# Performance work log

Measured on AMD Instinct MI355X. Metric: run time of the kernel, lower is better.

Reference implementation:

```python
import jax, jax.numpy as jnp
import numpy as np

B, S, E, H = 2, 2048, 1024, 16
D = E // H  # head dim = 64


def setup_inputs() -> dict:
    key = jax.random.key(0)
    ks = jax.random.split(key, 8)
    s = 1.0 / np.sqrt(E)  # keep projections well-scaled
    return {
        "query": jax.random.normal(ks[0], (B, S, E), jnp.float32),
        "key": jax.random.normal(ks[1], (B, S, E), jnp.float32),
        "value": jax.random.normal(ks[2], (B, S, E), jnp.float32),
        "Wq": jax.random.normal(ks[3], (E, E), jnp.float32) * s,
        "bq": jnp.zeros((E,), jnp.float32),
        "Wk": jax.random.normal(ks[4], (E, E), jnp.float32) * s,
        "bk": jnp.zeros((E,), jnp.float32),
        "Wv": jax.random.normal(ks[5], (E, E), jnp.float32) * s,
        "bv": jnp.zeros((E,), jnp.float32),
        "Wo": jax.random.normal(ks[6], (E, E), jnp.float32) * s,
        "bo": jnp.zeros((E,), jnp.float32),
    }


def _split_heads(x):
    # (b, s, h*d) -> (b, h, s, d)
    b, s, _ = x.shape
    return x.reshape(b, s, H, D).transpose(0, 2, 1, 3)


def reference(query, key, value, Wq, bq, Wk, bk, Wv, bv, Wo, bo):
    # Linear projections (torch Linear: x @ W^T + b)
    q = _split_heads(query @ Wq.T + bq)  # (b, h, s_q, d)
    k = _split_heads(key @ Wk.T + bk)    # (b, h, s_k, d)
    v = _split_heads(value @ Wv.T + bv)  # (b, h, s_k, d)
    # scaled dot-product attention; scale uses head dim of key
    scores = jnp.einsum("bhqd,bhkd->bhqk", q, k) * (D ** -0.5)
    attn = jax.nn.softmax(scores, axis=-1)  # (b, h, s_q, s_k)
    ctx = jnp.einsum("bhqk,bhkd->bhqd", attn, v)
    # merge heads: (b, h, s, d) -> (b, s, h*d)
    ctx = ctx.transpose(0, 2, 1, 3).reshape(B, S, H * D)
    out = ctx @ Wo.T + bo  # (b, s, out_dim)
    return out, attn
```

## Files before the change

### kernel.cpp

```cpp
#include <hip/hip_runtime.h>

typedef _Float16 f16;
typedef _Float16 f16x4 __attribute__((ext_vector_type(4)));
typedef _Float16 f16x8 __attribute__((ext_vector_type(8)));
typedef float f32x4 __attribute__((ext_vector_type(4)));

#define S_LEN 2048
#define EMB 1024
#define NH 16
#define HD 64
#define BATCH 2

__device__ __forceinline__ void gload_lds16(const void* g, void* l) {
  __builtin_amdgcn_global_load_lds(
      (const __attribute__((address_space(1))) void*)g,
      (__attribute__((address_space(3))) void*)l, 16, 0, 0);
}

__global__ __launch_bounds__(256) void cast_kernel(const float* __restrict__ in,
                                                   f16* __restrict__ out, int n4) {
  int i = blockIdx.x * 256 + threadIdx.x;
  if (i >= n4) return;
  const float4 v = reinterpret_cast<const float4*>(in)[i];
  f16x4 o;
  o[0] = (f16)v.x; o[1] = (f16)v.y; o[2] = (f16)v.z; o[3] = (f16)v.w;
  reinterpret_cast<f16x4*>(out)[i] = o;
}

template <int MODE>
__global__ __launch_bounds__(256) void gemm_bt(const f16* __restrict__ A,
                                               const f16* __restrict__ Bw,
                                               const float* __restrict__ bias,
                                               void* __restrict__ outp,
                                               int M, int N, int K) {
  __shared__ f16 As[128 * 64];
  __shared__ f16 Bs[64 * 64];
  const int tid = threadIdx.x;
  const int w = tid >> 6, lane = tid & 63;
  const int lg = lane >> 4, l15 = lane & 15;
  const int m0 = blockIdx.y * 128, n0 = blockIdx.x * 64;
  f32x4 acc[2][4] = {};
  for (int k0 = 0; k0 < K; k0 += 64) {
#pragma unroll
    for (int i = 0; i < 4; i++) {
      int c = i * 4 + w, o = c * 64 + lane;
      gload_lds16(A + (size_t)(m0 + (o >> 3)) * K + k0 + ((o & 7) << 3), As + c * 512);
    }
#pragma unroll
    for (int i = 0; i < 2; i++) {
      int c = i * 4 + w, o = c * 64 + lane;
      gload_lds16(Bw + (size_t)(n0 + (o >> 3)) * K + k0 + ((o & 7) << 3), Bs + c * 512);
    }
    __syncthreads();
#pragma unroll
    for (int kk = 0; kk < 2; kk++) {
      f16x8 af[2], bf[4];
#pragma unroll
      for (int mi = 0; mi < 2; mi++)
        af[mi] = *(const f16x8*)&As[(w * 32 + mi * 16 + l15) * 64 + kk * 32 + lg * 8];
#pragma unroll
      for (int ni = 0; ni < 4; ni++)
        bf[ni] = *(const f16x8*)&Bs[(ni * 16 + l15) * 64 + kk * 32 + lg * 8];
#pragma unroll
      for (int mi = 0; mi < 2; mi++)
#pragma unroll
        for (int ni = 0; ni < 4; ni++)
          acc[mi][ni] =
              __builtin_amdgcn_mfma_f32_16x16x32_f16(af[mi], bf[ni], acc[mi][ni], 0, 0, 0);
    }
    __syncthreads();
  }
#pragma unroll
  for (int mi = 0; mi < 2; mi++)
#pragma unroll
    for (int ni = 0; ni < 4; ni++) {
      const int gn = n0 + ni * 16 + l15;
      const float bv = bias[gn];
#pragma unroll
      for (int r = 0; r < 4; r++) {
        const int gm = m0 + w * 32 + mi * 16 + lg * 4 + r;
        const float v = acc[mi][ni][r] + bv;
        if (MODE == 1) {
          ((float*)outp)[(size_t)gm * N + gn] = v;
        } else {
          const int b = gm >> 11, s = gm & 2047;
          const int h = gn >> 6, d = gn & 63;
          if (MODE == 0)
            ((f16*)outp)[(((size_t)(b * NH + h)) * S_LEN + s) * HD + d] = (f16)v;
          else
            ((f16*)outp)[(((size_t)(b * NH + h)) * HD + d) * S_LEN + s] = (f16)v;
        }
      }
    }
}

__global__ __launch_bounds__(256) void attn_kernel(const f16* __restrict__ Qp,
                                                   const f16* __restrict__ Kp,
                                                   const f16* __restrict__ VtG,
                                                   float* __restrict__ attn_out,
                                                   f16* __restrict__ ctx_out) {
  __shared__ f16 Vt[64 * 128];
  __shared__ f16 Ps[4][16 * 136];
  const int tid = threadIdx.x;
  const int w = tid >> 6, lane = tid & 63;
  const int lg = lane >> 4, l15 = lane & 15;
  const int bh = blockIdx.y;
  const int b = bh >> 4, h = bh & 15;
  const int q0 = blockIdx.x * 64;
  const f16* Qbh = Qp + (size_t)bh * S_LEN * HD;
  const f16* Kbh = Kp + (size_t)bh * S_LEN * HD;
  const f16* Vtbh = VtG + (size_t)bh * HD * S_LEN;
  const int qrow_base = q0 + w * 16;

  f16x8 qf[2];
  const f16 qsc = (f16)0.18033688f;
#pragma unroll
  for (int kk = 0; kk < 2; kk++) {
    qf[kk] = *(const f16x8*)&Qbh[(size_t)(qrow_base + l15) * HD + kk * 32 + lg * 8];
#pragma unroll
    for (int j = 0; j < 8; j++) qf[kk][j] *= qsc;
  }

  float m2[4], l[4];
#pragma unroll
  for (int r = 0; r < 4; r++) { m2[r] = -1e30f; l[r] = 0.f; }

  for (int kt = 0; kt < S_LEN; kt += 128) {
    f32x4 sf[8] = {};
#pragma unroll
    for (int kk = 0; kk < 2; kk++)
#pragma unroll
      for (int nf = 0; nf < 8; nf++) {
        f16x8 kf = *(const f16x8*)&Kbh[(size_t)(kt + nf * 16 + l15) * HD + kk * 32 + lg * 8];
        sf[nf] = __builtin_amdgcn_mfma_f32_16x16x32_f16(qf[kk], kf, sf[nf], 0, 0, 0);
      }
#pragma unroll
    for (int r = 0; r < 4; r++) {
      float pm = sf[0][r];
#pragma unroll
      for (int nf = 1; nf < 8; nf++) pm = fmaxf(pm, sf[nf][r]);
#pragma unroll
      for (int ofs = 1; ofs < 16; ofs <<= 1) pm = fmaxf(pm, __shfl_xor(pm, ofs));
      const float mn = fmaxf(m2[r], pm);
      float ps = 0.f;
#pragma unroll
      for (int nf = 0; nf < 8; nf++) ps += exp2f(sf[nf][r] - mn);
#pragma unroll
      for (int ofs = 1; ofs < 16; ofs <<= 1) ps += __shfl_xor(ps, ofs);
      l[r] = l[r] * exp2f(m2[r] - mn) + ps;
      m2[r] = mn;
    }
  }
#pragma unroll
  for (int r = 0; r < 4; r++) m2[r] += log2f(l[r]);

#define STAGE_LOAD(KT)                                                      \
  {                                                                         \
    _Pragma("unroll") for (int c = 0; c < 4; c++) {                         \
      const int idx = c * 256 + tid;                                        \
      const int rr = idx >> 4, bb = idx & 15;                               \
      vreg[c] = *(const f16x8*)&Vtbh[(size_t)rr * S_LEN + (KT) + bb * 8];   \
    }                                                                       \
  }
#define STAGE_WRITE()                                                       \
  {                                                                         \
    _Pragma("unroll") for (int c = 0; c < 4; c++) {                         \
      const int idx = c * 256 + tid;                                        \
      const int rr = idx >> 4, bb = idx & 15;                               \
      *(f16x8*)((char*)Vt + rr * 256 + ((bb ^ (rr & 7)) << 4)) = vreg[c];   \
    }                                                                       \
  }

  f32x4 cacc[4] = {};
  f16x8 vreg[4];
  STAGE_LOAD(0);
  STAGE_WRITE();
  asm volatile("s_waitcnt lgkmcnt(0)\n\ts_barrier" ::: "memory");

  for (int t = 0; t < 16; t++) {
    const int kt = t * 128;
    STAGE_LOAD(((t + 1) & 15) * 128);

    f32x4 sf[8] = {};
#pragma unroll
    for (int kk = 0; kk < 2; kk++)
#pragma unroll
      for (int nf = 0; nf < 8; nf++) {
        f16x8 kf = *(const f16x8*)&Kbh[(size_t)(kt + nf * 16 + l15) * HD + kk * 32 + lg * 8];
        sf[nf] = __builtin_amdgcn_mfma_f32_16x16x32_f16(qf[kk], kf, sf[nf], 0, 0, 0);
      }
#pragma unroll
    for (int nf = 0; nf < 8; nf++)
#pragma unroll
      for (int r = 0; r < 4; r++) {
        const float p = exp2f(sf[nf][r] - m2[r]);
        const int qrow = qrow_base + lg * 4 + r;
        attn_out[((size_t)bh * S_LEN + qrow) * S_LEN + kt + nf * 16 + l15] = p;
        Ps[w][(lg * 4 + r) * 136 + nf * 16 + l15] = (f16)p;
      }
#pragma unroll
    for (int kk2 = 0; kk2 < 4; kk2++) {
      f16x8 pf = *(const f16x8*)&Ps[w][l15 * 136 + kk2 * 32 + lg * 8];
#pragma unroll
      for (int nf2 = 0; nf2 < 4; nf2++) {
        const int rr = nf2 * 16 + l15, bb = kk2 * 4 + lg;
        f16x8 vf = *(const f16x8*)((const char*)Vt + rr * 256 + ((bb ^ (rr & 7)) << 4));
        cacc[nf2] = __builtin_amdgcn_mfma_f32_16x16x32_f16(pf, vf, cacc[nf2], 0, 0, 0);
      }
    }
    asm volatile("s_barrier" ::: "memory");
    STAGE_WRITE();
    asm volatile("s_waitcnt lgkmcnt(0)\n\ts_barrier" ::: "memory");
  }
#pragma unroll
  for (int nf2 = 0; nf2 < 4; nf2++)
#pragma unroll
    for (int r = 0; r < 4; r++) {
      const int qrow = qrow_base + lg * 4 + r;
      const int gr = b * S_LEN + qrow;
      const int gc = h * HD + nf2 * 16 + l15;
      ctx_out[(size_t)gr * EMB + gc] = (f16)cacc[nf2][r];
    }
#undef STAGE_LOAD
#undef STAGE_WRITE
}

extern "C" void kernel_launch(void* const* d_in, const int* in_sizes, int n_in,
                              void* d_out, int out_size, void* d_ws, size_t ws_size,
                              hipStream_t stream) {
  const float* query = (const float*)d_in[0];
  const float* key_i = (const float*)d_in[1];
  const float* value = (const float*)d_in[2];
  const float* Wq = (const float*)d_in[3];
  const float* bq = (const float*)d_in[4];
  const float* Wk = (const float*)d_in[5];
  const float* bk = (const float*)d_in[6];
  const float* Wv = (const float*)d_in[7];
  const float* bv = (const float*)d_in[8];
  const float* Wo = (const float*)d_in[9];
  const float* bo = (const float*)d_in[10];

  float* out = (float*)d_out;
  float* attn = out + (size_t)BATCH * S_LEN * EMB;

  f16* ws = (f16*)d_ws;
  const size_t NTOK = (size_t)BATCH * S_LEN;
  f16* Qh = ws;
  f16* Kh = Qh + NTOK * EMB;
  f16* Vh = Kh + NTOK * EMB;
  f16* Wqh = Vh + NTOK * EMB;
  f16* Wkh = Wqh + (size_t)EMB * EMB;
  f16* Wvh = Wkh + (size_t)EMB * EMB;
  f16* Woh = Wvh + (size_t)EMB * EMB;
  f16* Qp = Woh + (size_t)EMB * EMB;
  f16* Kp = Qp + NTOK * EMB;
  f16* VtG = Kp + NTOK * EMB;
  f16* ctx = VtG + NTOK * EMB;

  const int n4_x = (int)(NTOK * EMB / 4);
  const int n4_w = (int)((size_t)EMB * EMB / 4);
  cast_kernel<<<n4_x / 256, 256, 0, stream>>>(query, Qh, n4_x);
  cast_kernel<<<n4_x / 256, 256, 0, stream>>>(key_i, Kh, n4_x);
  cast_kernel<<<n4_x / 256, 256, 0, stream>>>(value, Vh, n4_x);
  cast_kernel<<<n4_w / 256, 256, 0, stream>>>(Wq, Wqh, n4_w);
  cast_kernel<<<n4_w / 256, 256, 0, stream>>>(Wk, Wkh, n4_w);
  cast_kernel<<<n4_w / 256, 256, 0, stream>>>(Wv, Wvh, n4_w);
  cast_kernel<<<n4_w / 256, 256, 0, stream>>>(Wo, Woh, n4_w);

  dim3 ggrid(EMB / 64, (unsigned)(NTOK / 128));
  gemm_bt<0><<<ggrid, 256, 0, stream>>>(Qh, Wqh, bq, Qp, (int)NTOK, EMB, EMB);
  gemm_bt<0><<<ggrid, 256, 0, stream>>>(Kh, Wkh, bk, Kp, (int)NTOK, EMB, EMB);
  gemm_bt<2><<<ggrid, 256, 0, stream>>>(Vh, Wvh, bv, VtG, (int)NTOK, EMB, EMB);

  attn_kernel<<<dim3(S_LEN / 64, BATCH * NH), 256, 0, stream>>>(Qp, Kp, VtG, attn, ctx);

  gemm_bt<1><<<ggrid, 256, 0, stream>>>(ctx, Woh, bo, out, (int)NTOK, EMB, EMB);
}
```

Measured before the change: 970.1 us.

## Transpose score MFMA operands for vectorized attn writes and shrink GEMM tiles

The attention kernel swaps the MFMA operand order so each lane holds four consecutive key columns of one query row. This allows float4 stores of the attention matrix, packed f16x4 writes to the P staging buffer, and a softmax reduction with only two cross-lane shuffles. The GEMM tile shrinks from 128x64 to 64x64, doubling the grid, and the transposed V projection now writes packed f16x4 along the sequence axis. The smaller tile gives more blocks but less operand reuse per block.

```diff
diff --git a/kernel.cpp b/kernel.cpp
--- a/kernel.cpp
+++ b/kernel.cpp
@@ -33,65 +33,61 @@
                                                const float* __restrict__ bias,
                                                void* __restrict__ outp,
                                                int M, int N, int K) {
-  __shared__ f16 As[128 * 64];
+  __shared__ f16 As[64 * 64];
   __shared__ f16 Bs[64 * 64];
   const int tid = threadIdx.x;
   const int w = tid >> 6, lane = tid & 63;
   const int lg = lane >> 4, l15 = lane & 15;
-  const int m0 = blockIdx.y * 128, n0 = blockIdx.x * 64;
-  f32x4 acc[2][4] = {};
+  const int m0 = blockIdx.y * 64, n0 = blockIdx.x * 64;
+  f32x4 acc[4] = {};
   for (int k0 = 0; k0 < K; k0 += 64) {
 #pragma unroll
-    for (int i = 0; i < 4; i++) {
+    for (int i = 0; i < 2; i++) {
       int c = i * 4 + w, o = c * 64 + lane;
       gload_lds16(A + (size_t)(m0 + (o >> 3)) * K + k0 + ((o & 7) << 3), As + c * 512);
-    }
-#pragma unroll
-    for (int i = 0; i < 2; i++) {
-      int c = i * 4 + w, o = c * 64 + lane;
       gload_lds16(Bw + (size_t)(n0 + (o >> 3)) * K + k0 + ((o & 7) << 3), Bs + c * 512);
     }
     __syncthreads();
 #pragma unroll
     for (int kk = 0; kk < 2; kk++) {
-      f16x8 af[2], bf[4];
-#pragma unroll
-      for (int mi = 0; mi < 2; mi++)
-        af[mi] = *(const f16x8*)&As[(w * 32 + mi * 16 + l15) * 64 + kk * 32 + lg * 8];
+      f16x8 af = *(const f16x8*)&As[(w * 16 + l15) * 64 + kk * 32 + lg * 8];
+      f16x8 bf[4];
 #pragma unroll
       for (int ni = 0; ni < 4; ni++)
         bf[ni] = *(const f16x8*)&Bs[(ni * 16 + l15) * 64 + kk * 32 + lg * 8];
 #pragma unroll
-      for (int mi = 0; mi < 2; mi++)
-#pragma unroll
-        for (int ni = 0; ni < 4; ni++)
-          acc[mi][ni] =
-              __builtin_amdgcn_mfma_f32_16x16x32_f16(af[mi], bf[ni], acc[mi][ni], 0, 0, 0);
+      for (int ni = 0; ni < 4; ni++)
+        acc[ni] = __builtin_amdgcn_mfma_f32_16x16x32_f16(af, bf[ni], acc[ni], 0, 0, 0);
     }
     __syncthreads();
   }
 #pragma unroll
-  for (int mi = 0; mi < 2; mi++)
-#pragma unroll
-    for (int ni = 0; ni < 4; ni++) {
-      const int gn = n0 + ni * 16 + l15;
-      const float bv = bias[gn];
+  for (int ni = 0; ni < 4; ni++) {
+    const int gn = n0 + ni * 16 + l15;
+    const float bv = bias[gn];
+    if (MODE == 2) {
+      const int gm0 = m0 + w * 16 + lg * 4;
+      const int b = gm0 >> 11, s0 = gm0 & 2047;
+      const int h = gn >> 6, d = gn & 63;
+      f16x4 pk;
+#pragma unroll
+      for (int r = 0; r < 4; r++) pk[r] = (f16)(acc[ni][r] + bv);
+      *(f16x4*)&((f16*)outp)[(((size_t)(b * NH + h)) * HD + d) * S_LEN + s0] = pk;
+    } else {
 #pragma unroll
       for (int r = 0; r < 4; r++) {
-        const int gm = m0 + w * 32 + mi * 16 + lg * 4 + r;
-        const float v = acc[mi][ni][r] + bv;
+        const int gm = m0 + w * 16 + lg * 4 + r;
+        const float v = acc[ni][r] + bv;
         if (MODE == 1) {
           ((float*)outp)[(size_t)gm * N + gn] = v;
         } else {
           const int b = gm >> 11, s = gm & 2047;
           const int h = gn >> 6, d = gn & 63;
-          if (MODE == 0)
-            ((f16*)outp)[(((size_t)(b * NH + h)) * S_LEN + s) * HD + d] = (f16)v;
-          else
-            ((f16*)outp)[(((size_t)(b * NH + h)) * HD + d) * S_LEN + s] = (f16)v;
+          ((f16*)outp)[(((size_t)(b * NH + h)) * S_LEN + s) * HD + d] = (f16)v;
         }
       }
     }
+  }
 }
 
 __global__ __launch_bounds__(256) void attn_kernel(const f16* __restrict__ Qp,
@@ -110,20 +106,18 @@
   const f16* Qbh = Qp + (size_t)bh * S_LEN * HD;
   const f16* Kbh = Kp + (size_t)bh * S_LEN * HD;
   const f16* Vtbh = VtG + (size_t)bh * HD * S_LEN;
-  const int qrow_base = q0 + w * 16;
+  const int qrow = q0 + w * 16 + l15;
 
   f16x8 qf[2];
   const f16 qsc = (f16)0.18033688f;
 #pragma unroll
   for (int kk = 0; kk < 2; kk++) {
-    qf[kk] = *(const f16x8*)&Qbh[(size_t)(qrow_base + l15) * HD + kk * 32 + lg * 8];
+    qf[kk] = *(const f16x8*)&Qbh[(size_t)qrow * HD + kk * 32 + lg * 8];
 #pragma unroll
     for (int j = 0; j < 8; j++) qf[kk][j] *= qsc;
   }
 
-  float m2[4], l[4];
-#pragma unroll
-  for (int r = 0; r < 4; r++) { m2[r] = -1e30f; l[r] = 0.f; }
+  float m2 = -1e30f, l = 0.f;
 
   for (int kt = 0; kt < S_LEN; kt += 128) {
     f32x4 sf[8] = {};
@@ -132,27 +126,27 @@
 #pragma unroll
       for (int nf = 0; nf < 8; nf++) {
         f16x8 kf = *(const f16x8*)&Kbh[(size_t)(kt + nf * 16 + l15) * HD + kk * 32 + lg * 8];
-        sf[nf] = __builtin_amdgcn_mfma_f32_16x16x32_f16(qf[kk], kf, sf[nf], 0, 0, 0);
-      }
-#pragma unroll
-    for (int r = 0; r < 4; r++) {
-      float pm = sf[0][r];
-#pragma unroll
-      for (int nf = 1; nf < 8; nf++) pm = fmaxf(pm, sf[nf][r]);
-#pragma unroll
-      for (int ofs = 1; ofs < 16; ofs <<= 1) pm = fmaxf(pm, __shfl_xor(pm, ofs));
-      const float mn = fmaxf(m2[r], pm);
-      float ps = 0.f;
-#pragma unroll
-      for (int nf = 0; nf < 8; nf++) ps += exp2f(sf[nf][r] - mn);
-#pragma unroll
-      for (int ofs = 1; ofs < 16; ofs <<= 1) ps += __shfl_xor(ps, ofs);
-      l[r] = l[r] * exp2f(m2[r] - mn) + ps;
-      m2[r] = mn;
-    }
-  }
-#pragma unroll
-  for (int r = 0; r < 4; r++) m2[r] += log2f(l[r]);
+        sf[nf] = __builtin_amdgcn_mfma_f32_16x16x32_f16(kf, qf[kk], sf[nf], 0, 0, 0);
+      }
+    float pm = sf[0][0];
+#pragma unroll
+    for (int nf = 0; nf < 8; nf++)
+#pragma unroll
+      for (int r = 0; r < 4; r++) pm = fmaxf(pm, sf[nf][r]);
+    pm = fmaxf(pm, __shfl_xor(pm, 16));
+    pm = fmaxf(pm, __shfl_xor(pm, 32));
+    const float mn = fmaxf(m2, pm);
+    float ps = 0.f;
+#pragma unroll
+    for (int nf = 0; nf < 8; nf++)
+#pragma unroll
+      for (int r = 0; r < 4; r++) ps += exp2f(sf[nf][r] - mn);
+    ps += __shfl_xor(ps, 16);
+    ps += __shfl_xor(ps, 32);
+    l = l * exp2f(m2 - mn) + ps;
+    m2 = mn;
+  }
+  m2 += log2f(l);
 
 #define STAGE_LOAD(KT)                                                      \
   {                                                                         \
@@ -177,6 +171,8 @@
   STAGE_WRITE();
   asm volatile("s_waitcnt lgkmcnt(0)\n\ts_barrier" ::: "memory");
 
+  float* arow_base = attn_out + ((size_t)bh * S_LEN + qrow) * S_LEN + lg * 4;
+
   for (int t = 0; t < 16; t++) {
     const int kt = t * 128;
     STAGE_LOAD(((t + 1) & 15) * 128);
@@ -187,17 +183,20 @@
 #pragma unroll
       for (int nf = 0; nf < 8; nf++) {
         f16x8 kf = *(const f16x8*)&Kbh[(size_t)(kt + nf * 16 + l15) * HD + kk * 32 + lg * 8];
-        sf[nf] = __builtin_amdgcn_mfma_f32_16x16x32_f16(qf[kk], kf, sf[nf], 0, 0, 0);
-      }
-#pragma unroll
-    for (int nf = 0; nf < 8; nf++)
-#pragma unroll
-      for (int r = 0; r < 4; r++) {
-        const float p = exp2f(sf[nf][r] - m2[r]);
-        const int qrow = qrow_base + lg * 4 + r;
-        attn_out[((size_t)bh * S_LEN + qrow) * S_LEN + kt + nf * 16 + l15] = p;
-        Ps[w][(lg * 4 + r) * 136 + nf * 16 + l15] = (f16)p;
-      }
+        sf[nf] = __builtin_amdgcn_mfma_f32_16x16x32_f16(kf, qf[kk], sf[nf], 0, 0, 0);
+      }
+#pragma unroll
+    for (int nf = 0; nf < 8; nf++) {
+      float4 pv;
+      pv.x = exp2f(sf[nf][0] - m2);
+      pv.y = exp2f(sf[nf][1] - m2);
+      pv.z = exp2f(sf[nf][2] - m2);
+      pv.w = exp2f(sf[nf][3] - m2);
+      *(float4*)&arow_base[kt + nf * 16] = pv;
+      f16x4 ph;
+      ph[0] = (f16)pv.x; ph[1] = (f16)pv.y; ph[2] = (f16)pv.z; ph[3] = (f16)pv.w;
+      *(f16x4*)&Ps[w][l15 * 136 + nf * 16 + lg * 4] = ph;
+    }
 #pragma unroll
     for (int kk2 = 0; kk2 < 4; kk2++) {
       f16x8 pf = *(const f16x8*)&Ps[w][l15 * 136 + kk2 * 32 + lg * 8];
@@ -216,8 +215,8 @@
   for (int nf2 = 0; nf2 < 4; nf2++)
 #pragma unroll
     for (int r = 0; r < 4; r++) {
-      const int qrow = qrow_base + lg * 4 + r;
-      const int gr = b * S_LEN + qrow;
+      const int qr = q0 + w * 16 + lg * 4 + r;
+      const int gr = b * S_LEN + qr;
       const int gc = h * HD + nf2 * 16 + l15;
       ctx_out[(size_t)gr * EMB + gc] = (f16)cacc[nf2][r];
     }
@@ -267,7 +266,7 @@
   cast_kernel<<<n4_w / 256, 256, 0, stream>>>(Wv, Wvh, n4_w);
   cast_kernel<<<n4_w / 256, 256, 0, stream>>>(Wo, Woh, n4_w);
 
-  dim3 ggrid(EMB / 64, (unsigned)(NTOK / 128));
+  dim3 ggrid(EMB / 64, (unsigned)(NTOK / 64));
   gemm_bt<0><<<ggrid, 256, 0, stream>>>(Qh, Wqh, bq, Qp, (int)NTOK, EMB, EMB);
   gemm_bt<0><<<ggrid, 256, 0, stream>>>(Kh, Wkh, bk, Kp, (int)NTOK, EMB, EMB);
   gemm_bt<2><<<ggrid, 256, 0, stream>>>(Vh, Wvh, bv, VtG, (int)NTOK, EMB, EMB);
```

Measured after the change: 1.068 ms. 10.0% more time.

## Batch QKV projections into one launch with 128x128 GEMM tiles

Applied to the files above, without the earlier changes.

Replaces the 128x64 GEMM with a 128x128 tile kernel where each wave computes a 64x64 sub-tile, which doubles operand reuse per LDS load. The three Q/K/V projections become one launch, with the grid column index selecting the input, weight and output, so there are fewer launches and more blocks per launch. The transposed V output is now written as packed f16x4 vector stores. Each thread holds twice the accumulators, which raises register pressure and can lower occupancy. The output projection gets half as many blocks as before.

```diff
diff --git a/kernel.cpp b/kernel.cpp
--- a/kernel.cpp
+++ b/kernel.cpp
@@ -27,19 +27,31 @@
   reinterpret_cast<f16x4*>(out)[i] = o;
 }
 
-template <int MODE>
-__global__ __launch_bounds__(256) void gemm_bt(const f16* __restrict__ A,
-                                               const f16* __restrict__ Bw,
-                                               const float* __restrict__ bias,
-                                               void* __restrict__ outp,
-                                               int M, int N, int K) {
+template <int OUT>
+__global__ __launch_bounds__(256) void gemm128(
+    const f16* __restrict__ A0, const f16* __restrict__ A1, const f16* __restrict__ A2,
+    const f16* __restrict__ B0, const f16* __restrict__ B1, const f16* __restrict__ B2,
+    const float* __restrict__ b0, const float* __restrict__ b1, const float* __restrict__ b2,
+    void* o0, void* o1, void* o2, int K) {
   __shared__ f16 As[128 * 64];
-  __shared__ f16 Bs[64 * 64];
-  const int tid = threadIdx.x;
-  const int w = tid >> 6, lane = tid & 63;
+  __shared__ f16 Bs[128 * 64];
+  const int tid = threadIdx.x, w = tid >> 6, lane = tid & 63;
   const int lg = lane >> 4, l15 = lane & 15;
-  const int m0 = blockIdx.y * 128, n0 = blockIdx.x * 64;
-  f32x4 acc[2][4] = {};
+  const int wr = w >> 1, wc = w & 1;
+  const int m0 = blockIdx.y * 128;
+  const int n0g = blockIdx.x * 128;
+  const f16 *A, *Bw;
+  const float* bias;
+  int sel, n0;
+  if (OUT == 0) {
+    sel = n0g >> 10; n0 = n0g & 1023;
+    A = sel == 0 ? A0 : (sel == 1 ? A1 : A2);
+    Bw = sel == 0 ? B0 : (sel == 1 ? B1 : B2);
+    bias = sel == 0 ? b0 : (sel == 1 ? b1 : b2);
+  } else {
+    sel = 0; n0 = n0g; A = A0; Bw = B0; bias = b0;
+  }
+  f32x4 acc[4][4] = {};
   for (int k0 = 0; k0 < K; k0 += 64) {
 #pragma unroll
     for (int i = 0; i < 4; i++) {
@@ -47,22 +59,22 @@
       gload_lds16(A + (size_t)(m0 + (o >> 3)) * K + k0 + ((o & 7) << 3), As + c * 512);
     }
 #pragma unroll
-    for (int i = 0; i < 2; i++) {
+    for (int i = 0; i < 4; i++) {
       int c = i * 4 + w, o = c * 64 + lane;
       gload_lds16(Bw + (size_t)(n0 + (o >> 3)) * K + k0 + ((o & 7) << 3), Bs + c * 512);
     }
     __syncthreads();
 #pragma unroll
     for (int kk = 0; kk < 2; kk++) {
-      f16x8 af[2], bf[4];
-#pragma unroll
-      for (int mi = 0; mi < 2; mi++)
-        af[mi] = *(const f16x8*)&As[(w * 32 + mi * 16 + l15) * 64 + kk * 32 + lg * 8];
+      f16x8 af[4], bf[4];
+#pragma unroll
+      for (int mi = 0; mi < 4; mi++)
+        af[mi] = *(const f16x8*)&As[(wr * 64 + mi * 16 + l15) * 64 + kk * 32 + lg * 8];
 #pragma unroll
       for (int ni = 0; ni < 4; ni++)
-        bf[ni] = *(const f16x8*)&Bs[(ni * 16 + l15) * 64 + kk * 32 + lg * 8];
-#pragma unroll
-      for (int mi = 0; mi < 2; mi++)
+        bf[ni] = *(const f16x8*)&Bs[(wc * 64 + ni * 16 + l15) * 64 + kk * 32 + lg * 8];
+#pragma unroll
+      for (int mi = 0; mi < 4; mi++)
 #pragma unroll
         for (int ni = 0; ni < 4; ni++)
           acc[mi][ni] =
@@ -71,24 +83,30 @@
     __syncthreads();
   }
 #pragma unroll
-  for (int mi = 0; mi < 2; mi++)
+  for (int mi = 0; mi < 4; mi++)
 #pragma unroll
     for (int ni = 0; ni < 4; ni++) {
-      const int gn = n0 + ni * 16 + l15;
-      const float bv = bias[gn];
-#pragma unroll
-      for (int r = 0; r < 4; r++) {
-        const int gm = m0 + w * 32 + mi * 16 + lg * 4 + r;
-        const float v = acc[mi][ni][r] + bv;
-        if (MODE == 1) {
-          ((float*)outp)[(size_t)gm * N + gn] = v;
+      const int col = n0 + wc * 64 + ni * 16 + l15;
+      const float bv = bias[col];
+      const int gm0 = m0 + wr * 64 + mi * 16 + lg * 4;
+      if (OUT == 1) {
+#pragma unroll
+        for (int r = 0; r < 4; r++)
+          ((float*)o0)[(size_t)(gm0 + r) * EMB + col] = acc[mi][ni][r] + bv;
+      } else {
+        const int h = col >> 6, d = col & 63;
+        const int b = gm0 >> 11, s0 = gm0 & 2047;
+        if (sel == 2) {
+          f16x4 pk;
+#pragma unroll
+          for (int r = 0; r < 4; r++) pk[r] = (f16)(acc[mi][ni][r] + bv);
+          *(f16x4*)&((f16*)o2)[(((size_t)(b * NH + h)) * HD + d) * S_LEN + s0] = pk;
         } else {
-          const int b = gm >> 11, s = gm & 2047;
-          const int h = gn >> 6, d = gn & 63;
-          if (MODE == 0)
-            ((f16*)outp)[(((size_t)(b * NH + h)) * S_LEN + s) * HD + d] = (f16)v;
-          else
-            ((f16*)outp)[(((size_t)(b * NH + h)) * HD + d) * S_LEN + s] = (f16)v;
+          f16* op = sel == 0 ? (f16*)o0 : (f16*)o1;
+#pragma unroll
+          for (int r = 0; r < 4; r++)
+            op[(((size_t)(b * NH + h)) * S_LEN + s0 + r) * HD + d] =
+                (f16)(acc[mi][ni][r] + bv);
         }
       }
     }
@@ -267,12 +285,11 @@
   cast_kernel<<<n4_w / 256, 256, 0, stream>>>(Wv, Wvh, n4_w);
   cast_kernel<<<n4_w / 256, 256, 0, stream>>>(Wo, Woh, n4_w);
 
-  dim3 ggrid(EMB / 64, (unsigned)(NTOK / 128));
-  gemm_bt<0><<<ggrid, 256, 0, stream>>>(Qh, Wqh, bq, Qp, (int)NTOK, EMB, EMB);
-  gemm_bt<0><<<ggrid, 256, 0, stream>>>(Kh, Wkh, bk, Kp, (int)NTOK, EMB, EMB);
-  gemm_bt<2><<<ggrid, 256, 0, stream>>>(Vh, Wvh, bv, VtG, (int)NTOK, EMB, EMB);
+  gemm128<0><<<dim3(3 * EMB / 128, (unsigned)(NTOK / 128)), 256, 0, stream>>>(
+      Qh, Kh, Vh, Wqh, Wkh, Wvh, bq, bk, bv, Qp, Kp, VtG, EMB);
 
   attn_kernel<<<dim3(S_LEN / 64, BATCH * NH), 256, 0, stream>>>(Qp, Kp, VtG, attn, ctx);
 
-  gemm_bt<1><<<ggrid, 256, 0, stream>>>(ctx, Woh, bo, out, (int)NTOK, EMB, EMB);
-}
+  gemm128<1><<<dim3(EMB / 128, (unsigned)(NTOK / 128)), 256, 0, stream>>>(
+      ctx, ctx, ctx, Woh, Woh, Woh, bo, bo, bo, out, out, out, EMB);
+}
```

Result: no change. 973.3 us (+0.3%).
